# Performance work log

Measured on AMD Instinct MI355X. Metric: run time of the kernel, lower is better.

## Reference

```python
import jax, jax.numpy as jnp
import numpy as np

H = 256
N = 200000
B = 2048
M = 6


def _lstm_cell(x, h, c, Wih, Whh, bih, bhh):
    # PyTorch LSTM gate order: i, f, g, o
    gates = x @ Wih.T + h @ Whh.T + bih + bhh  # [B, 4H]
    i, f, g, o = jnp.split(gates, 4, axis=1)
    i = jax.nn.sigmoid(i)
    f = jax.nn.sigmoid(f)
    g = jnp.tanh(g)
    o = jax.nn.sigmoid(o)
    c_new = f * c + i * g
    h_new = o * jnp.tanh(c_new)
    return h_new, c_new


def setup_inputs() -> dict:
    key = jax.random.key(0)
    ks = jax.random.split(key, 11)
    s = 1.0 / np.sqrt(H)  # pytorch LSTM init scale
    nodes = jax.random.normal(ks[0], (N, H), jnp.float32)
    graph_id = jnp.sort(jax.random.randint(ks[1], (N,), 0, B, dtype=jnp.int64))
    return {
        "nodes": nodes,
        "graph_id": graph_id,
        "num_graphs": B,
        "Wih0": jax.random.normal(ks[2], (4 * H, 2 * H), jnp.float32) * s,
        "Whh0": jax.random.normal(ks[3], (4 * H, H), jnp.float32) * s,
        "bih0": jax.random.normal(ks[4], (4 * H,), jnp.float32) * s,
        "bhh0": jax.random.normal(ks[5], (4 * H,), jnp.float32) * s,
        "Wih1": jax.random.normal(ks[6], (4 * H, H), jnp.float32) * s,
        "Whh1": jax.random.normal(ks[7], (4 * H, H), jnp.float32) * s,
        "bih1": jax.random.normal(ks[8], (4 * H,), jnp.float32) * s,
        "bhh1": jax.random.normal(ks[9], (4 * H,), jnp.float32) * s,
    }


def reference(nodes, graph_id, num_graphs, Wih0, Whh0, bih0, bhh0, Wih1, Whh1, bih1, bhh1):
    n_hidden = nodes.shape[1]
    dt = nodes.dtype
    h0 = jnp.zeros((num_graphs, n_hidden), dt)
    c0 = jnp.zeros((num_graphs, n_hidden), dt)
    h1 = jnp.zeros((num_graphs, n_hidden), dt)
    c1 = jnp.zeros((num_graphs, n_hidden), dt)
    q = jnp.zeros((num_graphs, n_hidden), dt)
    q_star = None
    for i in range(M):
        # attention logits per node: e_v = <nodes_v, q_{g(v)}>
        e = jnp.sum(nodes * q[graph_id], axis=1)  # [N]
        # segment softmax over each graph
        emax = jax.ops.segment_max(e, graph_id, num_segments=num_graphs)
        ex = jnp.exp(e - emax[graph_id])
        denom = jax.ops.segment_sum(ex, graph_id, num_segments=num_graphs)
        a = ex / denom[graph_id]  # [N]
        # attention-weighted readout per graph
        r = jax.ops.segment_sum(a[:, None] * nodes, graph_id, num_segments=num_graphs)  # [B, H]
        q_star = jnp.concatenate([q, r], axis=1)  # [B, 2H]
        if i < M - 1:
            h0, c0 = _lstm_cell(q_star, h0, c0, Wih0, Whh0, bih0, bhh0)
            h1, c1 = _lstm_cell(h0, h1, c1, Wih1, Whh1, bih1, bhh1)
            q = h1
    return q_star
```

## Files before the change

### kernel.cpp

```cpp
#include <hip/hip_runtime.h>
#include <hip/hip_bf16.h>
#include <cstdint>

#define HDIM 256

typedef __attribute__((ext_vector_type(8))) short bf16x8;
typedef __attribute__((ext_vector_type(4))) float f32x4;

__device__ __forceinline__ float bf2f(unsigned short u) {
    union { unsigned u; float f; } v; v.u = ((unsigned)u) << 16; return v.f;
}
__device__ __forceinline__ unsigned short f2bf(float f) {
    union { float f; unsigned u; } v; v.f = f;
    unsigned u = v.u;
    return (unsigned short)((u + 0x7fffu + ((u >> 16) & 1u)) >> 16);
}
__device__ __forceinline__ void gload_lds16(const void* g, void* l) {
    __builtin_amdgcn_global_load_lds((const __attribute__((address_space(1))) void*)g,
                                     (__attribute__((address_space(3))) void*)l, 16, 0, 0);
}
__device__ __forceinline__ float fsigm(float x) {
    return 1.f / (1.f + __expf(-x));
}
__device__ __forceinline__ float ftanh(float x) {
    float ax = fabsf(x);
    float z = __expf(2.f * ax);
    float th = 1.f - 2.f / (z + 1.f);
    return copysignf(th, x);
}

__global__ void k_prep(const float* __restrict__ Wih0, const float* __restrict__ Whh0,
                       const float* __restrict__ bih0, const float* __restrict__ bhh0,
                       const float* __restrict__ Wih1, const float* __restrict__ Whh1,
                       const float* __restrict__ bih1, const float* __restrict__ bhh1,
                       unsigned short* __restrict__ W0, unsigned short* __restrict__ W1,
                       float* __restrict__ b0, float* __restrict__ b1,
                       const int* __restrict__ gid, int* __restrict__ offs, int N, int B) {
    int idx = blockIdx.x * 256 + threadIdx.x;
    const int n0 = 1024 * 768, n1 = 1024 * 512;
    if (idx < n0) {
        int r = idx / 768, k = idx - r * 768;
        int orow = ((r >> 4) & 3) * 256 + ((r >> 6) << 4) + (r & 15);
        float v = (k < 512) ? Wih0[orow * 512 + k] : Whh0[orow * 256 + (k - 512)];
        W0[idx] = f2bf(v);
    } else if (idx < n0 + n1) {
        int j = idx - n0;
        int r = j >> 9, k = j & 511;
        int orow = ((r >> 4) & 3) * 256 + ((r >> 6) << 4) + (r & 15);
        float v = (k < 256) ? Wih1[orow * 256 + k] : Whh1[orow * 256 + (k - 256)];
        W1[j] = f2bf(v);
    } else if (idx < n0 + n1 + 1024) {
        int r = idx - (n0 + n1);
        int orow = ((r >> 4) & 3) * 256 + ((r >> 6) << 4) + (r & 15);
        b0[r] = bih0[orow] + bhh0[orow];
        b1[r] = bih1[orow] + bhh1[orow];
    } else if (idx <= n0 + n1 + 1024 + B) {
        int g = idx - (n0 + n1 + 1024);
        int lo = 0, hi = N;
        while (lo < hi) { int mid = (lo + hi) >> 1; if (gid[mid] < g) lo = mid + 1; else hi = mid; }
        offs[g] = lo;
    }
}

template<bool BF>
__global__ void __launch_bounds__(256) k_mean_cast(const float* __restrict__ nodes,
                                                   const int* __restrict__ offs,
                                                   unsigned short* __restrict__ nbf,
                                                   unsigned short* __restrict__ xr,
                                                   unsigned short* __restrict__ xb1z,
                                                   float* __restrict__ c0,
                                                   float* __restrict__ c1, int N) {
    __shared__ float red[4 * HDIM];
    int g = blockIdx.x, t = threadIdx.x;
    int lane = t & 63, wid = t >> 6;
    int start = offs[g], end = offs[g + 1];
    int Nm1 = N - 1;
    size_t col = (size_t)lane * 4;
    float4 acc = {0.f, 0.f, 0.f, 0.f};
    for (int vi0 = start + wid * 4; vi0 < end; vi0 += 16) {
        float4 v[4];
#pragma unroll
        for (int r = 0; r < 4; ++r)
            v[r] = *(const float4*)(nodes + (size_t)min(vi0 + r, Nm1) * HDIM + col);
#pragma unroll
        for (int r = 0; r < 4; ++r) {
            if (vi0 + r < end) {
                acc.x += v[r].x; acc.y += v[r].y; acc.z += v[r].z; acc.w += v[r].w;
                if (BF) {
                    ushort4 o; o.x = f2bf(v[r].x); o.y = f2bf(v[r].y);
                    o.z = f2bf(v[r].z); o.w = f2bf(v[r].w);
                    *(ushort4*)(nbf + (size_t)(vi0 + r) * HDIM + col) = o;
                }
            }
        }
    }
    *(float4*)(red + wid * HDIM + lane * 4) = acc;
    __syncthreads();
    int n = end - start;
    float r = red[t] + red[HDIM + t] + red[2 * HDIM + t] + red[3 * HDIM + t];
    r = (n > 0) ? r / (float)n : 0.f;
    xr[(size_t)g * 768 + t] = 0;
    xr[(size_t)g * 768 + HDIM + t] = f2bf(r);
    xr[(size_t)g * 768 + 512 + t] = 0;
    xb1z[(size_t)g * 512 + 256 + t] = 0;
    c0[(size_t)g * HDIM + t] = 0.f;
    c1[(size_t)g * HDIM + t] = 0.f;
}

template<bool LAST>
__global__ void __launch_bounds__(256) k_attn(const unsigned short* __restrict__ nb,
                                              const int* __restrict__ offs,
                                              const float* __restrict__ q,
                                              float* __restrict__ out,
                                              unsigned short* __restrict__ xr, int N) {
    __shared__ float qs[HDIM];
    __shared__ float redr[8 * HDIM];
    __shared__ float redm[8], redd[8];
    int g = blockIdx.x, t = threadIdx.x;
    int lane = t & 63, wid = t >> 6;
    int half = lane >> 5, hl = lane & 31;
    int start = offs[g], end = offs[g + 1];
    int Nm1 = N - 1;
    float qv = q[(size_t)g * HDIM + t];
    qs[t] = qv;
    __syncthreads();
    float qv8[8];
#pragma unroll
    for (int j = 0; j < 8; ++j) qv8[j] = qs[hl * 8 + j];
    float m = -INFINITY, d = 0.f, racc[8];
#pragma unroll
    for (int j = 0; j < 8; ++j) racc[j] = 0.f;
    size_t col = (size_t)hl * 8;
    int vi0 = start + wid * 4;
    bf16x8 cura = *(const bf16x8*)(nb + (size_t)min(vi0 + half, Nm1) * HDIM + col);
    bf16x8 curb = *(const bf16x8*)(nb + (size_t)min(vi0 + 2 + half, Nm1) * HDIM + col);
    for (; vi0 < end; vi0 += 16) {
        int nvi = vi0 + 16;
        bf16x8 nxta = *(const bf16x8*)(nb + (size_t)min(nvi + half, Nm1) * HDIM + col);
        bf16x8 nxtb = *(const bf16x8*)(nb + (size_t)min(nvi + 2 + half, Nm1) * HDIM + col);
        int a = vi0 + half, b = a + 2;
        if (a < end) {
            float xa[8], xb[8];
#pragma unroll
            for (int j = 0; j < 8; ++j) {
                xa[j] = bf2f((unsigned short)cura[j]);
                xb[j] = bf2f((unsigned short)curb[j]);
            }
            float ea = 0.f, eb = 0.f;
#pragma unroll
            for (int j = 0; j < 8; ++j) {
                ea = fmaf(qv8[j], xa[j], ea);
                eb = fmaf(qv8[j], xb[j], eb);
            }
#pragma unroll
            for (int o = 16; o >= 1; o >>= 1) {
                ea += __shfl_xor(ea, o, 64);
                eb += __shfl_xor(eb, o, 64);
            }
            if (b >= end) eb = -INFINITY;
            float nm = fmaxf(fmaxf(m, ea), eb);
            float sc = __expf(m - nm);
            float wa = __expf(ea - nm);
            float wb = __expf(eb - nm);
            m = nm;
            d = fmaf(d, sc, wa + wb);
#pragma unroll
            for (int j = 0; j < 8; ++j)
                racc[j] = fmaf(racc[j], sc, fmaf(wa, xa[j], wb * xb[j]));
        }
        cura = nxta; curb = nxtb;
    }
    int g2 = wid * 2 + half;
    *(float4*)(redr + g2 * HDIM + hl * 8)     = (float4){racc[0], racc[1], racc[2], racc[3]};
    *(float4*)(redr + g2 * HDIM + hl * 8 + 4) = (float4){racc[4], racc[5], racc[6], racc[7]};
    if (hl == 0) { redm[g2] = m; redd[g2] = d; }
    __syncthreads();
    float M = -INFINITY;
#pragma unroll
    for (int i = 0; i < 8; ++i) M = fmaxf(M, redm[i]);
    float D = 0.f, R = 0.f;
#pragma unroll
    for (int i = 0; i < 8; ++i) {
        float s = (redm[i] == -INFINITY) ? 0.f : __expf(redm[i] - M);
        D += redd[i] * s;
        R += redr[i * HDIM + t] * s;
    }
    float r = (D > 0.f) ? R / D : 0.f;
    if (LAST) {
        size_t ob = (size_t)g * (2 * HDIM);
        out[ob + t] = qv;
        out[ob + HDIM + t] = r;
    } else {
        xr[(size_t)g * 768 + HDIM + t] = f2bf(r);
    }
}

template<bool LAST>
__global__ void __launch_bounds__(256) k_attn_f32(const float* __restrict__ nf,
                                                  const int* __restrict__ offs,
                                                  const float* __restrict__ q,
                                                  float* __restrict__ out,
                                                  unsigned short* __restrict__ xr) {
    __shared__ float qs[HDIM];
    __shared__ float redr[4 * HDIM];
    __shared__ float redm[4], redd[4];
    int g = blockIdx.x, t = threadIdx.x;
    int lane = t & 63, wid = t >> 6;
    int start = offs[g], end = offs[g + 1];
    float qv = q[(size_t)g * HDIM + t];
    qs[t] = qv;
    __syncthreads();
    float4 qq = *(const float4*)(qs + lane * 4);
    float m = -INFINITY, d = 0.f;
    float4 racc = {0.f, 0.f, 0.f, 0.f};
    for (int vi = start + wid; vi < end; vi += 4) {
        float4 x = *(const float4*)(nf + (size_t)vi * HDIM + lane * 4);
        float e = qq.x * x.x + qq.y * x.y + qq.z * x.z + qq.w * x.w;
#pragma unroll
        for (int o = 32; o >= 1; o >>= 1) e += __shfl_xor(e, o, 64);
        float nm = fmaxf(m, e);
        float sc = __expf(m - nm);
        float wv = __expf(e - nm);
        m = nm;
        d = d * sc + wv;
        racc.x = racc.x * sc + wv * x.x;
        racc.y = racc.y * sc + wv * x.y;
        racc.z = racc.z * sc + wv * x.z;
        racc.w = racc.w * sc + wv * x.w;
    }
    *(float4*)(redr + wid * HDIM + lane * 4) = racc;
    if (lane == 0) { redm[wid] = m; redd[wid] = d; }
    __syncthreads();
    float M = fmaxf(fmaxf(redm[0], redm[1]), fmaxf(redm[2], redm[3]));
    float D = 0.f, R = 0.f;
#pragma unroll
    for (int i = 0; i < 4; ++i) {
        float s = (redm[i] == -INFINITY) ? 0.f : __expf(redm[i] - M);
        D += redd[i] * s;
        R += redr[i * HDIM + t] * s;
    }
    float r = (D > 0.f) ? R / D : 0.f;
    if (LAST) {
        size_t ob = (size_t)g * (2 * HDIM);
        out[ob + t] = qv;
        out[ob + HDIM + t] = r;
    } else {
        xr[(size_t)g * 768 + HDIM + t] = f2bf(r);
    }
}

template<int K, int PHASE>
__global__ void __launch_bounds__(256) k_gemm_lstm(const unsigned short* __restrict__ A,
                                                   const unsigned short* __restrict__ W,
                                                   const float* __restrict__ bias_p,
                                                   float* __restrict__ c,
                                                   unsigned short* __restrict__ xa,
                                                   unsigned short* __restrict__ xb,
                                                   float* __restrict__ qout) {
    constexpr int BK = 64;
    constexpr int NT = K / BK;
    __shared__ unsigned short lA[3 * 64 * BK];
    __shared__ unsigned short lB[3 * 128 * BK];
    int t = threadIdx.x, lane = t & 63, wid = t >> 6;
    int wy = wid >> 1, wx = wid & 1;
    int brow = blockIdx.x * 64, bcol = blockIdx.y * 128;
    f32x4 acc[2][4];
#pragma unroll
    for (int i = 0; i < 2; ++i)
#pragma unroll
        for (int j = 0; j < 4; ++j) acc[i][j] = (f32x4){0.f, 0.f, 0.f, 0.f};
    const unsigned short* gA = A + (size_t)brow * K;
    const unsigned short* gW = W + (size_t)bcol * K;
    auto stage = [&](int tt, int b) {
        int k0 = tt * BK;
        unsigned short* dA = lA + b * (64 * BK);
        unsigned short* dB = lB + b * (128 * BK);
#pragma unroll
        for (int r = 0; r < 2; ++r) {
            int u = t + r * 256;
            int row = u >> 3, sc8 = (u & 7) ^ (row & 7);
            gload_lds16(gA + (size_t)row * K + k0 + sc8 * 8, dA + u * 8);
        }
#pragma unroll
        for (int r = 0; r < 4; ++r) {
            int u = t + r * 256;
            int row = u >> 3, sc8 = (u & 7) ^ (row & 7);
            gload_lds16(gW + (size_t)row * K + k0 + sc8 * 8, dB + u * 8);
        }
    };
    stage(0, 0);
    stage(1, 1);
    asm volatile("s_waitcnt vmcnt(6)" ::: "memory");
    __builtin_amdgcn_s_barrier();
    int arow = wy * 32 + (lane & 15);
    int brow2 = wx * 64 + (lane & 15);
    int gc8 = lane >> 4;
#pragma unroll
    for (int tt = 0; tt < NT; ++tt) {
        const unsigned short* bA = lA + (tt % 3) * (64 * BK);
        const unsigned short* bB = lB + (tt % 3) * (128 * BK);
        bf16x8 af[2][2], bfr[2][4];
#pragma unroll
        for (int kh = 0; kh < 2; ++kh) {
#pragma unroll
            for (int mm = 0; mm < 2; ++mm) {
                int row = arow + mm * 16;
                int ch = (gc8 + kh * 4) ^ (row & 7);
                af[kh][mm] = *(const bf16x8*)(bA + row * BK + ch * 8);
            }
#pragma unroll
            for (int nn = 0; nn < 4; ++nn) {
                int row = brow2 + nn * 16;
                int ch = (gc8 + kh * 4) ^ (row & 7);
                bfr[kh][nn] = *(const bf16x8*)(bB + row * BK + ch * 8);
            }
        }
        if (tt + 2 < NT) stage(tt + 2, (tt + 2) % 3);
#pragma unroll
        for (int kh = 0; kh < 2; ++kh)
#pragma unroll
            for (int mm = 0; mm < 2; ++mm)
#pragma unroll
                for (int nn = 0; nn < 4; ++nn)
                    acc[mm][nn] = __builtin_amdgcn_mfma_f32_16x16x32_bf16(
                        af[kh][mm], bfr[kh][nn], acc[mm][nn], 0, 0, 0);
        if (tt + 1 < NT) {
            if (tt + 2 < NT) asm volatile("s_waitcnt vmcnt(6)" ::: "memory");
            else             asm volatile("s_waitcnt vmcnt(0)" ::: "memory");
            __builtin_amdgcn_s_barrier();
        }
    }
    int f = lane & 15;
    int cg = bcol + wx * 64 + f;
    float bi = bias_p[cg], bff = bias_p[cg + 16], bg = bias_p[cg + 32], bo = bias_p[cg + 48];
    int feat = (blockIdx.y * 2 + wx) * 16 + f;
#pragma unroll
    for (int mm = 0; mm < 2; ++mm)
#pragma unroll
        for (int j = 0; j < 4; ++j) {
            int row = brow + wy * 32 + mm * 16 + (lane >> 4) * 4 + j;
            float gi = fsigm(acc[mm][0][j] + bi);
            float gf = fsigm(acc[mm][1][j] + bff);
            float gg = ftanh(acc[mm][2][j] + bg);
            float go = fsigm(acc[mm][3][j] + bo);
            size_t idx = (size_t)row * HDIM + feat;
            float cn_ = gf * c[idx] + gi * gg;
            c[idx] = cn_;
            float h = go * ftanh(cn_);
            unsigned short hb = f2bf(h);
            if (PHASE == 0) {
                xa[(size_t)row * 768 + 512 + feat] = hb;
                xb[(size_t)row * 512 + feat] = hb;
            } else {
                qout[idx] = h;
                xa[(size_t)row * 768 + feat] = hb;
                xb[(size_t)row * 512 + 256 + feat] = hb;
            }
        }
}

extern "C" void kernel_launch(void* const* d_in, const int* in_sizes, int n_in,
                              void* d_out, int out_size, void* d_ws, size_t ws_size,
                              hipStream_t stream) {
    const float* nodes = (const float*)d_in[0];
    const int* gid = (const int*)d_in[1];
    const float* Wih0 = (const float*)d_in[3];
    const float* Whh0 = (const float*)d_in[4];
    const float* bih0 = (const float*)d_in[5];
    const float* bhh0 = (const float*)d_in[6];
    const float* Wih1 = (const float*)d_in[7];
    const float* Whh1 = (const float*)d_in[8];
    const float* bih1 = (const float*)d_in[9];
    const float* bhh1 = (const float*)d_in[10];
    int N = in_sizes[0] / HDIM;
    int B = out_size / (2 * HDIM);
    float* out = (float*)d_out;

    const size_t AL = 512;
    auto rnd = [&](size_t b) { return (b + AL - 1) & ~(AL - 1); };
    size_t offs_b  = rnd((size_t)(B + 1) * 4);
    size_t q_b     = rnd((size_t)B * HDIM * 4);
    size_t xb0_b   = rnd((size_t)B * 768 * 2);
    size_t xb1_b   = rnd((size_t)B * 512 * 2);
    size_t w0_b    = rnd((size_t)1024 * 768 * 2);
    size_t w1_b    = rnd((size_t)1024 * 512 * 2);
    size_t bias_b  = rnd((size_t)1024 * 4);
    size_t nb_b    = rnd((size_t)N * HDIM * 2);
    size_t base_need = offs_b + 3 * q_b + 2 * xb0_b + 2 * xb1_b + w0_b + w1_b + 2 * bias_b;
    bool useBF = (base_need + nb_b <= ws_size);

    char* w = (char*)d_ws;
    unsigned short* nodes_bf = nullptr;
    if (useBF) { nodes_bf = (unsigned short*)w; w += nb_b; }
    int* offs = (int*)w;               w += offs_b;
    float* q  = (float*)w;             w += q_b;
    float* c0 = (float*)w;             w += q_b;
    float* c1 = (float*)w;             w += q_b;
    unsigned short* xb0v[2]; unsigned short* xb1v[2];
    xb0v[0] = (unsigned short*)w;      w += xb0_b;
    xb0v[1] = (unsigned short*)w;      w += xb0_b;
    xb1v[0] = (unsigned short*)w;      w += xb1_b;
    xb1v[1] = (unsigned short*)w;      w += xb1_b;
    unsigned short* W0 = (unsigned short*)w;  w += w0_b;
    unsigned short* W1 = (unsigned short*)w;  w += w1_b;
    float* b0 = (float*)w;             w += bias_b;
    float* b1 = (float*)w;             w += bias_b;

    {
        int total = 1024 * 768 + 1024 * 512 + 1024 + B + 1;
        k_prep<<<dim3((total + 255) / 256), dim3(256), 0, stream>>>(
            Wih0, Whh0, bih0, bhh0, Wih1, Whh1, bih1, bhh1, W0, W1, b0, b1,
            gid, offs, N, B);
    }
    if (useBF)
        k_mean_cast<true><<<dim3(B), dim3(256), 0, stream>>>(nodes, offs, nodes_bf,
                                                             xb0v[0], xb1v[0], c0, c1, N);
    else
        k_mean_cast<false><<<dim3(B), dim3(256), 0, stream>>>(nodes, offs, nullptr,
                                                              xb0v[0], xb1v[0], c0, c1, N);

    for (int s = 0; s < 5; ++s) {
        int vr = s & 1, vw = vr ^ 1;
        k_gemm_lstm<768, 0><<<dim3(B / 64, 8), dim3(256), 0, stream>>>(
            xb0v[vr], W0, b0, c0, xb0v[vw], xb1v[vr], nullptr);
        k_gemm_lstm<512, 1><<<dim3(B / 64, 8), dim3(256), 0, stream>>>(
            xb1v[vr], W1, b1, c1, xb0v[vw], xb1v[vw], q);
        if (s < 4) {
            if (useBF)
                k_attn<false><<<dim3(B), dim3(256), 0, stream>>>(nodes_bf, offs, q, nullptr, xb0v[vw], N);
            else
                k_attn_f32<false><<<dim3(B), dim3(256), 0, stream>>>(nodes, offs, q, nullptr, xb0v[vw]);
        } else {
            if (useBF)
                k_attn<true><<<dim3(B), dim3(256), 0, stream>>>(nodes_bf, offs, q, out, nullptr, N);
            else
                k_attn_f32<true><<<dim3(B), dim3(256), 0, stream>>>(nodes, offs, q, out, nullptr);
        }
    }
}
```

Baseline: 268.5 us.

## Fuse prep and mean-cast kernels; rework attention to 16 row-groups

Merges the weight/bias prep kernel and the mean/bf16-cast kernel into one launch. Mean blocks now compute their own segment offsets by binary search, so they no longer wait on the prep kernel. The attention kernel now assigns 16 lanes per node row, each lane covering 16 columns, giving 16 concurrent row groups per block instead of 8 pairs. This shortens the shuffle reduction and removes the two-row pairing, at the cost of more registers and a larger LDS reduction buffer.

```diff
diff --git a/kernel.cpp b/kernel.cpp
--- a/kernel.cpp
+++ b/kernel.cpp
@@ -29,14 +29,65 @@
     return copysignf(th, x);
 }
 
-__global__ void k_prep(const float* __restrict__ Wih0, const float* __restrict__ Whh0,
-                       const float* __restrict__ bih0, const float* __restrict__ bhh0,
-                       const float* __restrict__ Wih1, const float* __restrict__ Whh1,
-                       const float* __restrict__ bih1, const float* __restrict__ bhh1,
-                       unsigned short* __restrict__ W0, unsigned short* __restrict__ W1,
-                       float* __restrict__ b0, float* __restrict__ b1,
-                       const int* __restrict__ gid, int* __restrict__ offs, int N, int B) {
-    int idx = blockIdx.x * 256 + threadIdx.x;
+template<bool BF>
+__global__ void __launch_bounds__(256) k_prep_mean(
+        const float* __restrict__ nodes, const int* __restrict__ gid,
+        const float* __restrict__ Wih0, const float* __restrict__ Whh0,
+        const float* __restrict__ bih0, const float* __restrict__ bhh0,
+        const float* __restrict__ Wih1, const float* __restrict__ Whh1,
+        const float* __restrict__ bih1, const float* __restrict__ bhh1,
+        unsigned short* __restrict__ W0, unsigned short* __restrict__ W1,
+        float* __restrict__ b0, float* __restrict__ b1,
+        int* __restrict__ offs,
+        unsigned short* __restrict__ nbf, unsigned short* __restrict__ xr,
+        unsigned short* __restrict__ xb1z,
+        float* __restrict__ c0, float* __restrict__ c1, int N, int B) {
+    int bid = blockIdx.x;
+    int t = threadIdx.x;
+    if (bid < B) {
+        __shared__ float red[4 * HDIM];
+        int g = bid;
+        int lane = t & 63, wid = t >> 6;
+        int lo = 0, hi = N;
+        while (lo < hi) { int mid = (lo + hi) >> 1; if (gid[mid] < g) lo = mid + 1; else hi = mid; }
+        int start = lo;
+        hi = N;
+        while (lo < hi) { int mid = (lo + hi) >> 1; if (gid[mid] < g + 1) lo = mid + 1; else hi = mid; }
+        int end = lo;
+        int Nm1 = N - 1;
+        size_t col = (size_t)lane * 4;
+        float4 acc = {0.f, 0.f, 0.f, 0.f};
+        for (int vi0 = start + wid * 4; vi0 < end; vi0 += 16) {
+            float4 v[4];
+#pragma unroll
+            for (int r = 0; r < 4; ++r)
+                v[r] = *(const float4*)(nodes + (size_t)min(vi0 + r, Nm1) * HDIM + col);
+#pragma unroll
+            for (int r = 0; r < 4; ++r) {
+                if (vi0 + r < end) {
+                    acc.x += v[r].x; acc.y += v[r].y; acc.z += v[r].z; acc.w += v[r].w;
+                    if (BF) {
+                        ushort4 o; o.x = f2bf(v[r].x); o.y = f2bf(v[r].y);
+                        o.z = f2bf(v[r].z); o.w = f2bf(v[r].w);
+                        *(ushort4*)(nbf + (size_t)(vi0 + r) * HDIM + col) = o;
+                    }
+                }
+            }
+        }
+        *(float4*)(red + wid * HDIM + lane * 4) = acc;
+        __syncthreads();
+        int n = end - start;
+        float r = red[t] + red[HDIM + t] + red[2 * HDIM + t] + red[3 * HDIM + t];
+        r = (n > 0) ? r / (float)n : 0.f;
+        xr[(size_t)g * 768 + t] = 0;
+        xr[(size_t)g * 768 + HDIM + t] = f2bf(r);
+        xr[(size_t)g * 768 + 512 + t] = 0;
+        xb1z[(size_t)g * 512 + 256 + t] = 0;
+        c0[(size_t)g * HDIM + t] = 0.f;
+        c1[(size_t)g * HDIM + t] = 0.f;
+        return;
+    }
+    int idx = (bid - B) * 256 + t;
     const int n0 = 1024 * 768, n1 = 1024 * 512;
     if (idx < n0) {
         int r = idx / 768, k = idx - r * 768;
@@ -62,51 +113,6 @@
     }
 }
 
-template<bool BF>
-__global__ void __launch_bounds__(256) k_mean_cast(const float* __restrict__ nodes,
-                                                   const int* __restrict__ offs,
-                                                   unsigned short* __restrict__ nbf,
-                                                   unsigned short* __restrict__ xr,
-                                                   unsigned short* __restrict__ xb1z,
-                                                   float* __restrict__ c0,
-                                                   float* __restrict__ c1, int N) {
-    __shared__ float red[4 * HDIM];
-    int g = blockIdx.x, t = threadIdx.x;
-    int lane = t & 63, wid = t >> 6;
-    int start = offs[g], end = offs[g + 1];
-    int Nm1 = N - 1;
-    size_t col = (size_t)lane * 4;
-    float4 acc = {0.f, 0.f, 0.f, 0.f};
-    for (int vi0 = start + wid * 4; vi0 < end; vi0 += 16) {
-        float4 v[4];
-#pragma unroll
-        for (int r = 0; r < 4; ++r)
-            v[r] = *(const float4*)(nodes + (size_t)min(vi0 + r, Nm1) * HDIM + col);
-#pragma unroll
-        for (int r = 0; r < 4; ++r) {
-            if (vi0 + r < end) {
-                acc.x += v[r].x; acc.y += v[r].y; acc.z += v[r].z; acc.w += v[r].w;
-                if (BF) {
-                    ushort4 o; o.x = f2bf(v[r].x); o.y = f2bf(v[r].y);
-                    o.z = f2bf(v[r].z); o.w = f2bf(v[r].w);
-                    *(ushort4*)(nbf + (size_t)(vi0 + r) * HDIM + col) = o;
-                }
-            }
-        }
-    }
-    *(float4*)(red + wid * HDIM + lane * 4) = acc;
-    __syncthreads();
-    int n = end - start;
-    float r = red[t] + red[HDIM + t] + red[2 * HDIM + t] + red[3 * HDIM + t];
-    r = (n > 0) ? r / (float)n : 0.f;
-    xr[(size_t)g * 768 + t] = 0;
-    xr[(size_t)g * 768 + HDIM + t] = f2bf(r);
-    xr[(size_t)g * 768 + 512 + t] = 0;
-    xb1z[(size_t)g * 512 + 256 + t] = 0;
-    c0[(size_t)g * HDIM + t] = 0.f;
-    c1[(size_t)g * HDIM + t] = 0.f;
-}
-
 template<bool LAST>
 __global__ void __launch_bounds__(256) k_attn(const unsigned short* __restrict__ nb,
                                               const int* __restrict__ offs,
@@ -114,73 +120,66 @@
                                               float* __restrict__ out,
                                               unsigned short* __restrict__ xr, int N) {
     __shared__ float qs[HDIM];
-    __shared__ float redr[8 * HDIM];
-    __shared__ float redm[8], redd[8];
+    __shared__ float redr[16 * HDIM];
+    __shared__ float redm[16], redd[16];
     int g = blockIdx.x, t = threadIdx.x;
     int lane = t & 63, wid = t >> 6;
-    int half = lane >> 5, hl = lane & 31;
+    int qpos = lane & 15;
+    int gidx = wid * 4 + ((lane >> 4) & 3);
     int start = offs[g], end = offs[g + 1];
     int Nm1 = N - 1;
     float qv = q[(size_t)g * HDIM + t];
     qs[t] = qv;
     __syncthreads();
-    float qv8[8];
-#pragma unroll
-    for (int j = 0; j < 8; ++j) qv8[j] = qs[hl * 8 + j];
-    float m = -INFINITY, d = 0.f, racc[8];
-#pragma unroll
-    for (int j = 0; j < 8; ++j) racc[j] = 0.f;
-    size_t col = (size_t)hl * 8;
-    int vi0 = start + wid * 4;
-    bf16x8 cura = *(const bf16x8*)(nb + (size_t)min(vi0 + half, Nm1) * HDIM + col);
-    bf16x8 curb = *(const bf16x8*)(nb + (size_t)min(vi0 + 2 + half, Nm1) * HDIM + col);
-    for (; vi0 < end; vi0 += 16) {
-        int nvi = vi0 + 16;
-        bf16x8 nxta = *(const bf16x8*)(nb + (size_t)min(nvi + half, Nm1) * HDIM + col);
-        bf16x8 nxtb = *(const bf16x8*)(nb + (size_t)min(nvi + 2 + half, Nm1) * HDIM + col);
-        int a = vi0 + half, b = a + 2;
-        if (a < end) {
-            float xa[8], xb[8];
+    float qv16[16];
+#pragma unroll
+    for (int j = 0; j < 16; ++j) qv16[j] = qs[qpos * 16 + j];
+    float m = -INFINITY, d = 0.f, racc[16];
+#pragma unroll
+    for (int j = 0; j < 16; ++j) racc[j] = 0.f;
+    size_t col = (size_t)qpos * 16;
+    int niter = (end - start + 15) >> 4;
+    int vi = start + gidx;
+    bf16x8 curA = *(const bf16x8*)(nb + (size_t)min(vi, Nm1) * HDIM + col);
+    bf16x8 curB = *(const bf16x8*)(nb + (size_t)min(vi, Nm1) * HDIM + col + 8);
+    for (int it = 0; it < niter; ++it) {
+        int nvi = vi + 16;
+        bf16x8 nxtA = *(const bf16x8*)(nb + (size_t)min(nvi, Nm1) * HDIM + col);
+        bf16x8 nxtB = *(const bf16x8*)(nb + (size_t)min(nvi, Nm1) * HDIM + col + 8);
+        if (vi < end) {
+            float x[16];
 #pragma unroll
             for (int j = 0; j < 8; ++j) {
-                xa[j] = bf2f((unsigned short)cura[j]);
-                xb[j] = bf2f((unsigned short)curb[j]);
+                x[j] = bf2f((unsigned short)curA[j]);
+                x[8 + j] = bf2f((unsigned short)curB[j]);
             }
-            float ea = 0.f, eb = 0.f;
-#pragma unroll
-            for (int j = 0; j < 8; ++j) {
-                ea = fmaf(qv8[j], xa[j], ea);
-                eb = fmaf(qv8[j], xb[j], eb);
-            }
-#pragma unroll
-            for (int o = 16; o >= 1; o >>= 1) {
-                ea += __shfl_xor(ea, o, 64);
-                eb += __shfl_xor(eb, o, 64);
-            }
-            if (b >= end) eb = -INFINITY;
-            float nm = fmaxf(fmaxf(m, ea), eb);
+            float e = 0.f;
+#pragma unroll
+            for (int j = 0; j < 16; ++j) e = fmaf(qv16[j], x[j], e);
+#pragma unroll
+            for (int o = 8; o >= 1; o >>= 1) e += __shfl_xor(e, o, 64);
+            float nm = fmaxf(m, e);
             float sc = __expf(m - nm);
-            float wa = __expf(ea - nm);
-            float wb = __expf(eb - nm);
+            float w = __expf(e - nm);
             m = nm;
-            d = fmaf(d, sc, wa + wb);
-#pragma unroll
-            for (int j = 0; j < 8; ++j)
-                racc[j] = fmaf(racc[j], sc, fmaf(wa, xa[j], wb * xb[j]));
-        }
-        cura = nxta; curb = nxtb;
-    }
-    int g2 = wid * 2 + half;
-    *(float4*)(redr + g2 * HDIM + hl * 8)     = (float4){racc[0], racc[1], racc[2], racc[3]};
-    *(float4*)(redr + g2 * HDIM + hl * 8 + 4) = (float4){racc[4], racc[5], racc[6], racc[7]};
-    if (hl == 0) { redm[g2] = m; redd[g2] = d; }
+            d = fmaf(d, sc, w);
+#pragma unroll
+            for (int j = 0; j < 16; ++j) racc[j] = fmaf(racc[j], sc, w * x[j]);
+        }
+        vi = nvi; curA = nxtA; curB = nxtB;
+    }
+#pragma unroll
+    for (int j = 0; j < 16; j += 4)
+        *(float4*)(redr + gidx * HDIM + qpos * 16 + j) =
+            (float4){racc[j], racc[j + 1], racc[j + 2], racc[j + 3]};
+    if (qpos == 0) { redm[gidx] = m; redd[gidx] = d; }
     __syncthreads();
     float M = -INFINITY;
 #pragma unroll
-    for (int i = 0; i < 8; ++i) M = fmaxf(M, redm[i]);
+    for (int i = 0; i < 16; ++i) M = fmaxf(M, redm[i]);
     float D = 0.f, R = 0.f;
 #pragma unroll
-    for (int i = 0; i < 8; ++i) {
+    for (int i = 0; i < 16; ++i) {
         float s = (redm[i] == -INFINITY) ? 0.f : __expf(redm[i] - M);
         D += redd[i] * s;
         R += redr[i * HDIM + t] * s;
@@ -407,17 +406,18 @@
     float* b1 = (float*)w;             w += bias_b;
 
     {
-        int total = 1024 * 768 + 1024 * 512 + 1024 + B + 1;
-        k_prep<<<dim3((total + 255) / 256), dim3(256), 0, stream>>>(
-            Wih0, Whh0, bih0, bhh0, Wih1, Whh1, bih1, bhh1, W0, W1, b0, b1,
-            gid, offs, N, B);
-    }
-    if (useBF)
-        k_mean_cast<true><<<dim3(B), dim3(256), 0, stream>>>(nodes, offs, nodes_bf,
-                                                             xb0v[0], xb1v[0], c0, c1, N);
-    else
-        k_mean_cast<false><<<dim3(B), dim3(256), 0, stream>>>(nodes, offs, nullptr,
-                                                              xb0v[0], xb1v[0], c0, c1, N);
+        int prep_total = 1024 * 768 + 1024 * 512 + 1024 + B + 1;
+        int prep_blocks = (prep_total + 255) / 256;
+        dim3 grid(B + prep_blocks);
+        if (useBF)
+            k_prep_mean<true><<<grid, dim3(256), 0, stream>>>(
+                nodes, gid, Wih0, Whh0, bih0, bhh0, Wih1, Whh1, bih1, bhh1,
+                W0, W1, b0, b1, offs, nodes_bf, xb0v[0], xb1v[0], c0, c1, N, B);
+        else
+            k_prep_mean<false><<<grid, dim3(256), 0, stream>>>(
+                nodes, gid, Wih0, Whh0, bih0, bhh0, Wih1, Whh1, bih1, bhh1,
+                W0, W1, b0, b1, offs, nullptr, xb0v[0], xb1v[0], c0, c1, N, B);
+    }
 
     for (int s = 0; s < 5; ++s) {
         int vr = s & 1, vw = vr ^ 1;
```

Measured after the change: 273.3 us. No clear change (+1.8%).
